# Kernel tuning notes

Hardware: AMD Instinct MI355X
Metric: run time of the kernel (lower is better)

The kernel has to match this reference:

```python
import jax, jax.numpy as jnp
import numpy as np

T, B, E, H = 256, 8, 512, 32
EXP = 512            # number of expanded (periodic-image) keys
SMOOTH = 20.0        # smooth_factor


def setup_inputs() -> dict:
    key = jax.random.key(0)
    ks = jax.random.split(key, 12)
    s = 1.0 / np.sqrt(E)
    return {
        "query": jax.random.normal(ks[0], (T, B, E), dtype=jnp.float32),
        "outcell_index": jax.random.randint(ks[1], (B, EXP), 0, T),
        "expand_mask": jax.random.bernoulli(ks[2], 0.1, (B, EXP)),
        "key_padding_mask": jax.random.bernoulli(ks[3], 0.1, (B, T)),
        "local_attention_weight": jax.random.uniform(ks[4], (B, T, T + EXP), dtype=jnp.float32),
        "Wq": jax.random.normal(ks[5], (E, E), dtype=jnp.float32) * s,
        "bq": jnp.zeros((E,), dtype=jnp.float32),
        "Wk": jax.random.normal(ks[6], (E, E), dtype=jnp.float32) * s,   # k_bias=False
        "Wv": jax.random.normal(ks[7], (E, E), dtype=jnp.float32) * s,
        "bv": jnp.zeros((E,), dtype=jnp.float32),
        "Wo": jax.random.normal(ks[8], (E, E), dtype=jnp.float32) * s,
        "bo": jnp.zeros((E,), dtype=jnp.float32),
    }


def reference(query, outcell_index, expand_mask, key_padding_mask,
              local_attention_weight, Wq, bq, Wk, Wv, bv, Wo, bo):
    t, b, e = query.shape
    hd = e // H
    # QKV projections (torch Linear: y = x @ W.T + b)
    q = jnp.einsum('tbe,fe->tbf', query, Wq) + bq
    k = jnp.einsum('tbe,fe->tbf', query, Wk)          # no k bias
    v = jnp.einsum('tbe,fe->tbf', query, Wv) + bv
    # PBC gather-expand K/V along the time axis
    oc = outcell_index.T[:, :, None]                  # [EXP, B, 1]
    k = jnp.concatenate([k, jnp.take_along_axis(k, oc, axis=0)], axis=0)  # [S,B,E]
    v = jnp.concatenate([v, jnp.take_along_axis(v, oc, axis=0)], axis=0)
    s_len = k.shape[0]
    # [len, B, E] -> [B, H, len, hd]
    qh = q.reshape(t, b, H, hd).transpose(1, 2, 0, 3)
    kh = k.reshape(s_len, b, H, hd).transpose(1, 2, 0, 3)
    vh = v.reshape(s_len, b, H, hd).transpose(1, 2, 0, 3)
    # NOTE: forward() never applies self.scaling in this path (faithful)
    scores = jnp.einsum('bhtd,bhsd->bhts', qh, kh)    # [B,H,T,S]
    law = local_attention_weight[:, None]             # [B,1,T,S]
    scores = (scores + SMOOTH) * law - SMOOTH         # smooth softmax
    kpm = jnp.concatenate([key_padding_mask, expand_mask], axis=1)  # [B,S]
    scores = jnp.where(kpm[:, None, None, :], -jnp.inf, scores)
    probs = jax.nn.softmax(scores, axis=-1)
    probs = probs * law                               # post-softmax reweight
    attn = jnp.einsum('bhts,bhsd->bhtd', probs, vh)   # [B,H,T,hd]
    attn = attn.transpose(2, 0, 1, 3).reshape(t, b, e)
    return jnp.einsum('tbe,fe->tbf', attn, Wo) + bo
```

## Files before the change

kernel.cpp:

```cpp
#include <hip/hip_runtime.h>
#include <stdint.h>

#define T_ 256
#define B_ 8
#define E_ 512
#define H_ 32
#define HD_ 16
#define EXP_ 512
#define S_ 768
#define M_ 2048
#define SMOOTH_ 20.0f
#define PSTR 36
#define VSTR 800

typedef __attribute__((ext_vector_type(8)))  short bf16x8;
typedef __attribute__((ext_vector_type(4)))  float f32x4;
typedef __attribute__((ext_vector_type(16))) float f32x16;

__device__ __forceinline__ unsigned int pk2(float a, float b)
{
    unsigned int ua = __float_as_uint(a);
    ua = ua + 0x7FFFu + ((ua >> 16) & 1u);
    unsigned int ub = __float_as_uint(b);
    ub = ub + 0x7FFFu + ((ub >> 16) & 1u);
    return (ua >> 16) | (ub & 0xFFFF0000u);
}
__device__ __forceinline__ ushort bf1(float a)
{
    unsigned int u = __float_as_uint(a);
    u = u + 0x7FFFu + ((u >> 16) & 1u);
    return (ushort)(u >> 16);
}

union U16 { uint4 u; bf16x8 v; };

__device__ __forceinline__ void mfma_gemm_body(const float* __restrict__ X,
                                               const float* __restrict__ W,
                                               int m0, int n0,
                                               f32x4 acc[2][2],
                                               ushort* As, ushort* Bs)
{
    const int tid  = threadIdx.x;
    const int lrow = tid >> 2;
    const int kq   = tid & 3;
    const int l    = tid & 63;
    const int w    = tid >> 6;
    const int wm   = w & 1;
    const int wn   = w >> 1;
    const int lq   = l >> 4;
    const int ln   = l & 15;

    const float* Xr = &X[(size_t)(m0 + lrow) * E_ + kq * 16];
    const float* Wr = &W[(size_t)(n0 + lrow) * E_ + kq * 16];
    ushort* Aw = &As[lrow * 72 + kq * 16];
    ushort* Bw = &Bs[lrow * 72 + kq * 16];

    for (int k0 = 0; k0 < E_; k0 += 64) {
        float4 a0 = *(const float4*)&Xr[k0 + 0];
        float4 a1 = *(const float4*)&Xr[k0 + 4];
        float4 a2 = *(const float4*)&Xr[k0 + 8];
        float4 a3 = *(const float4*)&Xr[k0 + 12];
        float4 b0 = *(const float4*)&Wr[k0 + 0];
        float4 b1 = *(const float4*)&Wr[k0 + 4];
        float4 b2 = *(const float4*)&Wr[k0 + 8];
        float4 b3 = *(const float4*)&Wr[k0 + 12];

        uint4 ua0 = make_uint4(pk2(a0.x, a0.y), pk2(a0.z, a0.w),
                               pk2(a1.x, a1.y), pk2(a1.z, a1.w));
        uint4 ua1 = make_uint4(pk2(a2.x, a2.y), pk2(a2.z, a2.w),
                               pk2(a3.x, a3.y), pk2(a3.z, a3.w));
        uint4 ub0 = make_uint4(pk2(b0.x, b0.y), pk2(b0.z, b0.w),
                               pk2(b1.x, b1.y), pk2(b1.z, b1.w));
        uint4 ub1 = make_uint4(pk2(b2.x, b2.y), pk2(b2.z, b2.w),
                               pk2(b3.x, b3.y), pk2(b3.z, b3.w));

        __syncthreads();
        *(uint4*)&Aw[0] = ua0;
        *(uint4*)&Aw[8] = ua1;
        *(uint4*)&Bw[0] = ub0;
        *(uint4*)&Bw[8] = ub1;
        __syncthreads();

#pragma unroll
        for (int kb = 0; kb < 2; ++kb) {
            bf16x8 af0 = *(const bf16x8*)&As[(32 * wm + ln) * 72 + 32 * kb + lq * 8];
            bf16x8 af1 = *(const bf16x8*)&As[(32 * wm + 16 + ln) * 72 + 32 * kb + lq * 8];
            bf16x8 bf0 = *(const bf16x8*)&Bs[(32 * wn + ln) * 72 + 32 * kb + lq * 8];
            bf16x8 bf1 = *(const bf16x8*)&Bs[(32 * wn + 16 + ln) * 72 + 32 * kb + lq * 8];
            acc[0][0] = __builtin_amdgcn_mfma_f32_16x16x32_bf16(af0, bf0, acc[0][0], 0, 0, 0);
            acc[0][1] = __builtin_amdgcn_mfma_f32_16x16x32_bf16(af0, bf1, acc[0][1], 0, 0, 0);
            acc[1][0] = __builtin_amdgcn_mfma_f32_16x16x32_bf16(af1, bf0, acc[1][0], 0, 0, 0);
            acc[1][1] = __builtin_amdgcn_mfma_f32_16x16x32_bf16(af1, bf1, acc[1][1], 0, 0, 0);
        }
    }
}

__global__ __launch_bounds__(256)
void qkv_gemm(const float* __restrict__ X,
              const float* __restrict__ Wq, const float* __restrict__ bq,
              const float* __restrict__ Wk,
              const float* __restrict__ Wv, const float* __restrict__ bv,
              float* __restrict__ Q, float* __restrict__ K, float* __restrict__ V)
{
    __shared__ __align__(16) ushort As[64 * 72];
    __shared__ __align__(16) ushort Bs[64 * 72];
    const int z = blockIdx.z;
    const float* W    = (z == 0) ? Wq : (z == 1 ? Wk : Wv);
    const float* bias = (z == 0) ? bq : (z == 1 ? nullptr : bv);
    float* dst        = (z == 0) ? Q  : (z == 1 ? K  : V);
    const int rows    = (z == 0) ? T_ : S_;

    const int m0 = blockIdx.y * 64;
    const int n0 = blockIdx.x * 64;

    f32x4 acc[2][2];
#pragma unroll
    for (int i = 0; i < 2; ++i)
#pragma unroll
        for (int j = 0; j < 2; ++j)
            acc[i][j] = (f32x4){0.f, 0.f, 0.f, 0.f};

    mfma_gemm_body(X, W, m0, n0, acc, As, Bs);

    const int l  = threadIdx.x & 63;
    const int w  = threadIdx.x >> 6;
    const int wm = w & 1;
    const int wn = w >> 1;
    const int lq = l >> 4;
    const int ln = l & 15;

#pragma unroll
    for (int j = 0; j < 2; ++j) {
        const int nb = n0 + 32 * wn + 16 * j;
        const int h  = nb >> 4;
        const float bv_ = bias ? bias[nb + ln] : 0.f;
#pragma unroll
        for (int i = 0; i < 2; ++i) {
#pragma unroll
            for (int r = 0; r < 4; ++r) {
                const int m = m0 + 32 * wm + 16 * i + lq * 4 + r;
                const int t = m >> 3;
                const int b = m & 7;
                dst[(((size_t)(b * H_ + h)) * rows + t) * HD_ + ln] = acc[i][j][r] + bv_;
            }
        }
    }
}

__global__ __launch_bounds__(256)
void out_gemm(const float* __restrict__ X, const float* __restrict__ Wo,
              const float* __restrict__ bo, float* __restrict__ dst)
{
    __shared__ __align__(16) ushort As[64 * 72];
    __shared__ __align__(16) ushort Bs[64 * 72];
    const int m0 = blockIdx.y * 64;
    const int n0 = blockIdx.x * 64;

    f32x4 acc[2][2];
#pragma unroll
    for (int i = 0; i < 2; ++i)
#pragma unroll
        for (int j = 0; j < 2; ++j)
            acc[i][j] = (f32x4){0.f, 0.f, 0.f, 0.f};

    mfma_gemm_body(X, Wo, m0, n0, acc, As, Bs);

    const int l  = threadIdx.x & 63;
    const int w  = threadIdx.x >> 6;
    const int wm = w & 1;
    const int wn = w >> 1;
    const int lq = l >> 4;
    const int ln = l & 15;

#pragma unroll
    for (int j = 0; j < 2; ++j) {
        const int nb = n0 + 32 * wn + 16 * j;
        const float bo_ = bo[nb + ln];
#pragma unroll
        for (int i = 0; i < 2; ++i) {
#pragma unroll
            for (int r = 0; r < 4; ++r) {
                const int m = m0 + 32 * wm + 16 * i + lq * 4 + r;
                dst[(size_t)m * E_ + nb + ln] = acc[i][j][r] + bo_;
            }
        }
    }
}

__global__ __launch_bounds__(256)
void gather_kernel(const int* __restrict__ oc,
                   float* __restrict__ Kb, float* __restrict__ Vb)
{
    const int bj  = blockIdx.x;
    const int b   = bj >> 9;
    const int j   = bj & 511;
    const int src = oc[bj];

    const int tid   = threadIdx.x;
    const int which = tid >> 7;
    const int i     = tid & 127;
    const int h     = i >> 2;
    const int f4    = i & 3;
    float* P = which ? Vb : Kb;
    const float4* s4 = (const float4*)&P[(((size_t)(b * H_ + h)) * S_ + src) * HD_];
    float4*       d4 = (float4*)&P[(((size_t)(b * H_ + h)) * S_ + T_ + j) * HD_];
    d4[f4] = s4[f4];
}

__global__ __launch_bounds__(256)
void attn_kernel(const float* __restrict__ Q, const float* __restrict__ Kb,
                 const float* __restrict__ Vb, const float* __restrict__ LAW,
                 const int* __restrict__ kpm, const int* __restrict__ em,
                 float* __restrict__ A)
{
    __shared__ __align__(16) ushort Ks[S_ * HD_];
    __shared__ __align__(16) ushort Vt[HD_ * VSTR];
    __shared__ __align__(16) float  msf[S_];
    __shared__ __align__(16) float  Zbuf[128];
    __shared__ __align__(16) ushort Pb[4][32 * PSTR];

    const int tid    = threadIdx.x;
    const int blk    = blockIdx.x;
    const int bh     = blk >> 1;
    const int thalf  = blk & 1;
    const int b      = bh >> 5;
    const int h      = bh & 31;

    {
        const float4* src = (const float4*)&Kb[(size_t)bh * S_ * HD_];
        for (int f = tid; f < S_ * HD_ / 4; f += 256) {
            float4 v = src[f];
            *(uint2*)&Ks[f * 4] = make_uint2(pk2(v.x, v.y), pk2(v.z, v.w));
        }
    }
    for (int s = tid; s < S_; s += 256) {
        const float* vr = &Vb[((size_t)bh * S_ + s) * HD_];
#pragma unroll
        for (int d = 0; d < 16; ++d)
            Vt[d * VSTR + s] = bf1(vr[d]);
    }
    for (int s = tid; s < S_; s += 256) {
        int m = (s < T_) ? kpm[b * T_ + s] : em[b * EXP_ + (s - T_)];
        msf[s] = m ? 0.f : 1.f;
    }

    const int w      = tid >> 6;
    const int l      = tid & 63;
    const int tloc   = l & 31;
    const int khalf  = l >> 5;
    const int tglob  = thalf * 128 + w * 32 + tloc;
    bf16x8 qf;
    {
        const float* qp = &Q[((size_t)bh * T_ + tglob) * HD_ + khalf * 8];
        float4 q0 = *(const float4*)qp;
        float4 q1 = *(const float4*)(qp + 4);
        U16 u;
        u.u = make_uint4(pk2(q0.x, q0.y), pk2(q0.z, q0.w),
                         pk2(q1.x, q1.y), pk2(q1.z, q1.w));
        qf = u.v;
    }

    __syncthreads();

    const f32x16 zero16 = {0.f,0.f,0.f,0.f,0.f,0.f,0.f,0.f,
                           0.f,0.f,0.f,0.f,0.f,0.f,0.f,0.f};
    f32x4 o0 = {0.f, 0.f, 0.f, 0.f};
    f32x4 o1 = {0.f, 0.f, 0.f, 0.f};
    float Z = 0.f;

    const float* lawp = &LAW[((size_t)b * T_ + tglob) * S_];
    ushort* prow = &Pb[w][tloc * PSTR];
    const int tl = l & 15;
    const int kg = l >> 4;

    for (int i = 0; i < S_ / 32; ++i) {
        bf16x8 kf = *(const bf16x8*)&Ks[(i * 32 + tloc) * HD_ + khalf * 8];
        f32x16 sc = __builtin_amdgcn_mfma_f32_32x32x16_bf16(kf, qf, zero16, 0, 0, 0);

#pragma unroll
        for (int qd = 0; qd < 4; ++qd) {
            const int sb = i * 32 + qd * 8 + khalf * 4;
            float4 mf = *(const float4*)&msf[sb];
            float4 lw = *(const float4*)&lawp[sb];
            float e0, e1, e2, e3;
            {
                float x = (sc[qd*4+0] + SMOOTH_) * lw.x - SMOOTH_;
                e0 = mf.x * __expf(x - 50.f);
                x = (sc[qd*4+1] + SMOOTH_) * lw.y - SMOOTH_;
                e1 = mf.y * __expf(x - 50.f);
                x = (sc[qd*4+2] + SMOOTH_) * lw.z - SMOOTH_;
                e2 = mf.z * __expf(x - 50.f);
                x = (sc[qd*4+3] + SMOOTH_) * lw.w - SMOOTH_;
                e3 = mf.w * __expf(x - 50.f);
            }
            Z += (e0 + e1) + (e2 + e3);
            *(uint2*)&prow[qd * 8 + khalf * 4] =
                make_uint2(pk2(e0 * lw.x, e1 * lw.y), pk2(e2 * lw.z, e3 * lw.w));
        }

        bf16x8 vf = *(const bf16x8*)&Vt[tl * VSTR + i * 32 + kg * 8];

        {
            const ushort* pr0 = &Pb[w][(0 * 16 + tl) * PSTR + kg * 8];
            U16 u;
            uint2 a0 = *(const uint2*)pr0;
            uint2 a1 = *(const uint2*)(pr0 + 4);
            u.u = make_uint4(a0.x, a0.y, a1.x, a1.y);
            o0 = __builtin_amdgcn_mfma_f32_16x16x32_bf16(vf, u.v, o0, 0, 0, 0);
            const ushort* pr1 = &Pb[w][(1 * 16 + tl) * PSTR + kg * 8];
            uint2 b0 = *(const uint2*)pr1;
            uint2 b1 = *(const uint2*)(pr1 + 4);
            u.u = make_uint4(b0.x, b0.y, b1.x, b1.y);
            o1 = __builtin_amdgcn_mfma_f32_16x16x32_bf16(vf, u.v, o1, 0, 0, 0);
        }
    }

    Z += __shfl_xor(Z, 32);
    if (l < 32) Zbuf[w * 32 + tloc] = Z;
    __syncthreads();

#pragma unroll
    for (int th = 0; th < 2; ++th) {
        const float Zt  = Zbuf[w * 32 + th * 16 + tl];
        const float inv = (Zt > 0.f) ? 1.f / Zt : 0.f;
        const int   t   = thalf * 128 + w * 32 + th * 16 + tl;
        const f32x4 o   = th ? o1 : o0;
#pragma unroll
        for (int r = 0; r < 4; ++r) {
            const int d = kg * 4 + r;
            A[((size_t)t * B_ + b) * E_ + h * HD_ + d] = o[r] * inv;
        }
    }
}

extern "C" void kernel_launch(void* const* d_in, const int* in_sizes, int n_in,
                              void* d_out, int out_size, void* d_ws, size_t ws_size,
                              hipStream_t stream)
{
    const float* query = (const float*)d_in[0];
    const int*   oc    = (const int*)d_in[1];
    const int*   em    = (const int*)d_in[2];
    const int*   kpm   = (const int*)d_in[3];
    const float* law   = (const float*)d_in[4];
    const float* Wq    = (const float*)d_in[5];
    const float* bq    = (const float*)d_in[6];
    const float* Wk    = (const float*)d_in[7];
    const float* Wv    = (const float*)d_in[8];
    const float* bv    = (const float*)d_in[9];
    const float* Wo    = (const float*)d_in[10];
    const float* bo    = (const float*)d_in[11];
    float* out = (float*)d_out;

    float* ws = (float*)d_ws;
    float* Q = ws;
    float* K = Q + (size_t)1048576;
    float* V = K + (size_t)3145728;
    float* A = V + (size_t)3145728;

    dim3 gq(E_ / 64, M_ / 64, 3);
    qkv_gemm<<<gq, 256, 0, stream>>>(query, Wq, bq, Wk, Wv, bv, Q, K, V);

    gather_kernel<<<B_ * EXP_, 256, 0, stream>>>(oc, K, V);

    attn_kernel<<<B_ * H_ * 2, 256, 0, stream>>>(Q, K, V, law, kpm, em, A);

    dim3 go(E_ / 64, M_ / 64, 1);
    out_gemm<<<go, 256, 0, stream>>>(A, Wo, bo, out);
}
```

Measured before the change: 149.8 us.

## Store intermediates in bf16, fuse PBC gather into attention, pre-convert inputs

```diff
diff --git a/kernel.cpp b/kernel.cpp
--- a/kernel.cpp
+++ b/kernel.cpp
@@ -34,11 +34,38 @@
 
 union U16 { uint4 u; bf16x8 v; };
 
-__device__ __forceinline__ void mfma_gemm_body(const float* __restrict__ X,
-                                               const float* __restrict__ W,
-                                               int m0, int n0,
-                                               f32x4 acc[2][2],
-                                               ushort* As, ushort* Bs)
+__global__ __launch_bounds__(256)
+void conv_kernel(const float* __restrict__ X,
+                 const float* __restrict__ Wq, const float* __restrict__ Wk,
+                 const float* __restrict__ Wv, const float* __restrict__ Wo,
+                 ushort* __restrict__ Xb, ushort* __restrict__ Wb)
+{
+    const int seg = blockIdx.x >> 6;
+    const int blk = blockIdx.x & 63;
+    const float* src;
+    ushort* dst;
+    if (seg < 4) { src = X + (size_t)seg * 262144; dst = Xb + (size_t)seg * 262144; }
+    else {
+        const float* ws_[4] = {Wq, Wk, Wv, Wo};
+        src = ws_[seg - 4];
+        dst = Wb + (size_t)(seg - 4) * 262144;
+    }
+    const int base = blk * 4096 + threadIdx.x * 16;
+    float4 f0 = *(const float4*)&src[base + 0];
+    float4 f1 = *(const float4*)&src[base + 4];
+    float4 f2 = *(const float4*)&src[base + 8];
+    float4 f3 = *(const float4*)&src[base + 12];
+    *(uint4*)&dst[base + 0] = make_uint4(pk2(f0.x, f0.y), pk2(f0.z, f0.w),
+                                         pk2(f1.x, f1.y), pk2(f1.z, f1.w));
+    *(uint4*)&dst[base + 8] = make_uint4(pk2(f2.x, f2.y), pk2(f2.z, f2.w),
+                                         pk2(f3.x, f3.y), pk2(f3.z, f3.w));
+}
+
+__device__ __forceinline__ void mfma_gemm_body_bf(const ushort* __restrict__ X,
+                                                  const ushort* __restrict__ W,
+                                                  int m0, int n0,
+                                                  f32x4 acc[2][2],
+                                                  ushort* As, ushort* Bs)
 {
     const int tid  = threadIdx.x;
     const int lrow = tid >> 2;
@@ -50,37 +77,22 @@
     const int lq   = l >> 4;
     const int ln   = l & 15;
 
-    const float* Xr = &X[(size_t)(m0 + lrow) * E_ + kq * 16];
-    const float* Wr = &W[(size_t)(n0 + lrow) * E_ + kq * 16];
+    const ushort* Xr = &X[(size_t)(m0 + lrow) * E_ + kq * 16];
+    const ushort* Wr = &W[(size_t)(n0 + lrow) * E_ + kq * 16];
     ushort* Aw = &As[lrow * 72 + kq * 16];
     ushort* Bw = &Bs[lrow * 72 + kq * 16];
 
     for (int k0 = 0; k0 < E_; k0 += 64) {
-        float4 a0 = *(const float4*)&Xr[k0 + 0];
-        float4 a1 = *(const float4*)&Xr[k0 + 4];
-        float4 a2 = *(const float4*)&Xr[k0 + 8];
-        float4 a3 = *(const float4*)&Xr[k0 + 12];
-        float4 b0 = *(const float4*)&Wr[k0 + 0];
-        float4 b1 = *(const float4*)&Wr[k0 + 4];
-        float4 b2 = *(const float4*)&Wr[k0 + 8];
-        float4 b3 = *(const float4*)&Wr[k0 + 12];
-
-        uint4 ua0 = make_uint4(pk2(a0.x, a0.y), pk2(a0.z, a0.w),
-                               pk2(a1.x, a1.y), pk2(a1.z, a1.w));
-        uint4 ua1 = make_uint4(pk2(a2.x, a2.y), pk2(a2.z, a2.w),
-                               pk2(a3.x, a3.y), pk2(a3.z, a3.w));
-        uint4 ub0 = make_uint4(pk2(b0.x, b0.y), pk2(b0.z, b0.w),
-                               pk2(b1.x, b1.y), pk2(b1.z, b1.w));
-        uint4 ub1 = make_uint4(pk2(b2.x, b2.y), pk2(b2.z, b2.w),
-                               pk2(b3.x, b3.y), pk2(b3.z, b3.w));
-
+        uint4 a0 = *(const uint4*)&Xr[k0 + 0];
+        uint4 a1 = *(const uint4*)&Xr[k0 + 8];
+        uint4 b0 = *(const uint4*)&Wr[k0 + 0];
+        uint4 b1 = *(const uint4*)&Wr[k0 + 8];
         __syncthreads();
-        *(uint4*)&Aw[0] = ua0;
-        *(uint4*)&Aw[8] = ua1;
-        *(uint4*)&Bw[0] = ub0;
-        *(uint4*)&Bw[8] = ub1;
+        *(uint4*)&Aw[0] = a0;
+        *(uint4*)&Aw[8] = a1;
+        *(uint4*)&Bw[0] = b0;
+        *(uint4*)&Bw[8] = b1;
         __syncthreads();
-
 #pragma unroll
         for (int kb = 0; kb < 2; ++kb) {
             bf16x8 af0 = *(const bf16x8*)&As[(32 * wm + ln) * 72 + 32 * kb + lq * 8];
@@ -96,19 +108,16 @@
 }
 
 __global__ __launch_bounds__(256)
-void qkv_gemm(const float* __restrict__ X,
-              const float* __restrict__ Wq, const float* __restrict__ bq,
-              const float* __restrict__ Wk,
-              const float* __restrict__ Wv, const float* __restrict__ bv,
-              float* __restrict__ Q, float* __restrict__ K, float* __restrict__ V)
+void qkv_gemm(const ushort* __restrict__ Xb, const ushort* __restrict__ Wb,
+              const float* __restrict__ bq, const float* __restrict__ bv,
+              ushort* __restrict__ Qb, ushort* __restrict__ Kb,
+              ushort* __restrict__ VTb)
 {
     __shared__ __align__(16) ushort As[64 * 72];
     __shared__ __align__(16) ushort Bs[64 * 72];
     const int z = blockIdx.z;
-    const float* W    = (z == 0) ? Wq : (z == 1 ? Wk : Wv);
-    const float* bias = (z == 0) ? bq : (z == 1 ? nullptr : bv);
-    float* dst        = (z == 0) ? Q  : (z == 1 ? K  : V);
-    const int rows    = (z == 0) ? T_ : S_;
+    const ushort* W    = Wb + (size_t)z * 262144;
+    const float*  bias = (z == 0) ? bq : (z == 2 ? bv : nullptr);
 
     const int m0 = blockIdx.y * 64;
     const int n0 = blockIdx.x * 64;
@@ -120,7 +129,7 @@
         for (int j = 0; j < 2; ++j)
             acc[i][j] = (f32x4){0.f, 0.f, 0.f, 0.f};
 
-    mfma_gemm_body(X, W, m0, n0, acc, As, Bs);
+    mfma_gemm_body_bf(Xb, W, m0, n0, acc, As, Bs);
 
     const int l  = threadIdx.x & 63;
     const int w  = threadIdx.x >> 6;
@@ -133,6 +142,7 @@
     for (int j = 0; j < 2; ++j) {
         const int nb = n0 + 32 * wn + 16 * j;
         const int h  = nb >> 4;
+        const int d  = ln;
         const float bv_ = bias ? bias[nb + ln] : 0.f;
 #pragma unroll
         for (int i = 0; i < 2; ++i) {
@@ -141,14 +151,18 @@
                 const int m = m0 + 32 * wm + 16 * i + lq * 4 + r;
                 const int t = m >> 3;
                 const int b = m & 7;
-                dst[(((size_t)(b * H_ + h)) * rows + t) * HD_ + ln] = acc[i][j][r] + bv_;
+                const int bh = b * H_ + h;
+                const ushort val = bf1(acc[i][j][r] + bv_);
+                if (z == 0)      Qb[((size_t)bh * T_ + t) * HD_ + d] = val;
+                else if (z == 1) Kb[((size_t)bh * T_ + t) * HD_ + d] = val;
+                else             VTb[((size_t)bh * HD_ + d) * T_ + t] = val;
             }
         }
     }
 }
 
 __global__ __launch_bounds__(256)
-void out_gemm(const float* __restrict__ X, const float* __restrict__ Wo,
+void out_gemm(const ushort* __restrict__ Ab, const ushort* __restrict__ Wob,
               const float* __restrict__ bo, float* __restrict__ dst)
 {
     __shared__ __align__(16) ushort As[64 * 72];
@@ -163,7 +177,7 @@
         for (int j = 0; j < 2; ++j)
             acc[i][j] = (f32x4){0.f, 0.f, 0.f, 0.f};
 
-    mfma_gemm_body(X, Wo, m0, n0, acc, As, Bs);
+    mfma_gemm_body_bf(Ab, Wob, m0, n0, acc, As, Bs);
 
     const int l  = threadIdx.x & 63;
     const int w  = threadIdx.x >> 6;
@@ -188,30 +202,10 @@
 }
 
 __global__ __launch_bounds__(256)
-void gather_kernel(const int* __restrict__ oc,
-                   float* __restrict__ Kb, float* __restrict__ Vb)
-{
-    const int bj  = blockIdx.x;
-    const int b   = bj >> 9;
-    const int j   = bj & 511;
-    const int src = oc[bj];
-
-    const int tid   = threadIdx.x;
-    const int which = tid >> 7;
-    const int i     = tid & 127;
-    const int h     = i >> 2;
-    const int f4    = i & 3;
-    float* P = which ? Vb : Kb;
-    const float4* s4 = (const float4*)&P[(((size_t)(b * H_ + h)) * S_ + src) * HD_];
-    float4*       d4 = (float4*)&P[(((size_t)(b * H_ + h)) * S_ + T_ + j) * HD_];
-    d4[f4] = s4[f4];
-}
-
-__global__ __launch_bounds__(256)
-void attn_kernel(const float* __restrict__ Q, const float* __restrict__ Kb,
-                 const float* __restrict__ Vb, const float* __restrict__ LAW,
+void attn_kernel(const ushort* __restrict__ Qb, const ushort* __restrict__ Kb,
+                 const ushort* __restrict__ VTb, const float* __restrict__ LAW,
                  const int* __restrict__ kpm, const int* __restrict__ em,
-                 float* __restrict__ A)
+                 const int* __restrict__ oc, ushort* __restrict__ Ab)
 {
     __shared__ __align__(16) ushort Ks[S_ * HD_];
     __shared__ __align__(16) ushort Vt[HD_ * VSTR];
@@ -227,21 +221,40 @@
     const int h      = bh & 31;
 
     {
-        const float4* src = (const float4*)&Kb[(size_t)bh * S_ * HD_];
-        for (int f = tid; f < S_ * HD_ / 4; f += 256) {
-            float4 v = src[f];
-            *(uint2*)&Ks[f * 4] = make_uint2(pk2(v.x, v.y), pk2(v.z, v.w));
-        }
-    }
-    for (int s = tid; s < S_; s += 256) {
-        const float* vr = &Vb[((size_t)bh * S_ + s) * HD_];
-#pragma unroll
-        for (int d = 0; d < 16; ++d)
-            Vt[d * VSTR + s] = bf1(vr[d]);
-    }
-    for (int s = tid; s < S_; s += 256) {
-        int m = (s < T_) ? kpm[b * T_ + s] : em[b * EXP_ + (s - T_)];
-        msf[s] = m ? 0.f : 1.f;
+        const uint4* src = (const uint4*)&Kb[(size_t)bh * T_ * HD_];
+        uint4* dst = (uint4*)Ks;
+        dst[tid]       = src[tid];
+        dst[tid + 256] = src[tid + 256];
+    }
+    {
+#pragma unroll
+        for (int it = 0; it < 2; ++it) {
+            const int f = tid + it * 256;
+            const int row = f >> 5, ch = f & 31;
+            *(uint4*)&Vt[row * VSTR + ch * 8] =
+                *(const uint4*)&VTb[((size_t)bh * HD_ + row) * T_ + ch * 8];
+        }
+    }
+    {
+#pragma unroll
+        for (int it = 0; it < 2; ++it) {
+            const int j = tid + it * 256;
+            const int src = oc[b * EXP_ + j];
+            const uint4* kr = (const uint4*)&Kb[((size_t)bh * T_ + src) * HD_];
+            *(uint4*)&Ks[(T_ + j) * HD_ + 0] = kr[0];
+            *(uint4*)&Ks[(T_ + j) * HD_ + 8] = kr[1];
+#pragma unroll
+            for (int d = 0; d < 16; ++d)
+                Vt[d * VSTR + T_ + j] = VTb[((size_t)bh * HD_ + d) * T_ + src];
+        }
+    }
+    {
+#pragma unroll
+        for (int it = 0; it < 3; ++it) {
+            const int s = tid + it * 256;
+            const int m = (s < T_) ? kpm[b * T_ + s] : em[b * EXP_ + (s - T_)];
+            msf[s] = m ? 0.f : 1.f;
+        }
     }
 
     const int w      = tid >> 6;
@@ -249,16 +262,7 @@
     const int tloc   = l & 31;
     const int khalf  = l >> 5;
     const int tglob  = thalf * 128 + w * 32 + tloc;
-    bf16x8 qf;
-    {
-        const float* qp = &Q[((size_t)bh * T_ + tglob) * HD_ + khalf * 8];
-        float4 q0 = *(const float4*)qp;
-        float4 q1 = *(const float4*)(qp + 4);
-        U16 u;
-        u.u = make_uint4(pk2(q0.x, q0.y), pk2(q0.z, q0.w),
-                         pk2(q1.x, q1.y), pk2(q1.z, q1.w));
-        qf = u.v;
-    }
+    bf16x8 qf = *(const bf16x8*)&Qb[((size_t)bh * T_ + tglob) * HD_ + khalf * 8];
 
     __syncthreads();
 
@@ -299,7 +303,6 @@
         }
 
         bf16x8 vf = *(const bf16x8*)&Vt[tl * VSTR + i * 32 + kg * 8];
-
         {
             const ushort* pr0 = &Pb[w][(0 * 16 + tl) * PSTR + kg * 8];
             U16 u;
@@ -328,7 +331,7 @@
 #pragma unroll
         for (int r = 0; r < 4; ++r) {
             const int d = kg * 4 + r;
-            A[((size_t)t * B_ + b) * E_ + h * HD_ + d] = o[r] * inv;
+            Ab[((size_t)t * B_ + b) * E_ + h * HD_ + d] = bf1(o[r] * inv);
         }
     }
 }
@@ -351,19 +354,20 @@
     const float* bo    = (const float*)d_in[11];
     float* out = (float*)d_out;
 
-    float* ws = (float*)d_ws;
-    float* Q = ws;
-    float* K = Q + (size_t)1048576;
-    float* V = K + (size_t)3145728;
-    float* A = V + (size_t)3145728;
+    ushort* Xb  = (ushort*)d_ws;
+    ushort* Wb  = Xb  + (size_t)1048576;
+    ushort* Qb  = Wb  + (size_t)1048576;
+    ushort* Kb  = Qb  + (size_t)1048576;
+    ushort* VTb = Kb  + (size_t)1048576;
+    ushort* Ab  = VTb + (size_t)1048576;
+
+    conv_kernel<<<512, 256, 0, stream>>>(query, Wq, Wk, Wv, Wo, Xb, Wb);
 
     dim3 gq(E_ / 64, M_ / 64, 3);
-    qkv_gemm<<<gq, 256, 0, stream>>>(query, Wq, bq, Wk, Wv, bv, Q, K, V);
-
-    gather_kernel<<<B_ * EXP_, 256, 0, stream>>>(oc, K, V);
-
-    attn_kernel<<<B_ * H_ * 2, 256, 0, stream>>>(Q, K, V, law, kpm, em, A);
+    qkv_gemm<<<gq, 256, 0, stream>>>(Xb, Wb, bq, bv, Qb, Kb, VTb);
+
+    attn_kernel<<<B_ * H_ * 2, 256, 0, stream>>>(Qb, Kb, VTb, law, kpm, em, oc, Ab);
 
     dim3 go(E_ / 64, M_ / 64, 1);
-    out_gemm<<<go, 256, 0, stream>>>(A, Wo, bo, out);
-}
+    out_gemm<<<go, 256, 0, stream>>>(Ab, Wb + (size_t)3 * 262144, bo, out);
+}
```

Result: faster. 130.1 us (-13.2%).
